# Kernel optimization log

Measured on AMD Instinct MI355X. Metric: run time of the kernel, lower is better.

Reference implementation:

```python
import jax, jax.numpy as jnp
import numpy as np

N_NODES = 50000


def setup_inputs() -> dict:
    key = jax.random.key(0)
    ks = jax.random.split(key, 12)
    node_features = jax.random.normal(ks[0], (50000, 256), dtype=jnp.float32)
    hedge_features = jax.random.normal(ks[1], (25000, 128), dtype=jnp.float32)
    node_senders = jax.random.randint(ks[2], (800000,), 0, 50000, dtype=jnp.int32)
    node_receivers = jnp.sort(jax.random.randint(ks[3], (800000,), 0, 50000, dtype=jnp.int32))
    node_convolution = jax.random.uniform(ks[4], (800000, 1), dtype=jnp.float32)
    hedge2node_senders = jax.random.randint(ks[5], (400000,), 0, 25000, dtype=jnp.int32)
    hedge2node_receivers = jnp.sort(jax.random.randint(ks[6], (400000,), 0, 50000, dtype=jnp.int32))
    hedge2node_convolution = jax.random.uniform(ks[7], (400000, 1), dtype=jnp.float32)
    # Linear params (flax convention: y = x @ W + b, W is [in, out])
    W_msg = jax.random.normal(ks[8], (256, 256), dtype=jnp.float32) / np.sqrt(256.0)
    b_msg = jax.random.normal(ks[9], (256,), dtype=jnp.float32) * 0.01
    W_scale = jax.random.normal(ks[10], (128, 256), dtype=jnp.float32) / np.sqrt(128.0)
    b_scale = jax.random.normal(ks[11], (256,), dtype=jnp.float32) * 0.01
    return {
        "node_features": node_features,
        "hedge_features": hedge_features,
        "node_senders": node_senders,
        "node_receivers": node_receivers,
        "node_convolution": node_convolution,
        "hedge2node_senders": hedge2node_senders,
        "hedge2node_receivers": hedge2node_receivers,
        "hedge2node_convolution": hedge2node_convolution,
        "W_msg": W_msg,
        "b_msg": b_msg,
        "W_scale": W_scale,
        "b_scale": b_scale,
    }


def reference(node_features, hedge_features, node_senders, node_receivers,
              node_convolution, hedge2node_senders, hedge2node_receivers,
              hedge2node_convolution, W_msg, b_msg, W_scale, b_scale):
    # node -> node message pipeline: gather, Linear, per-edge scale, segment_sum
    sender_features = node_features[node_senders]                     # [E, Fin]
    messages = sender_features @ W_msg + b_msg                        # [E, Fout]
    scaled_messages = node_convolution * messages                     # [E, Fout]
    gathered_messages = jax.ops.segment_sum(
        scaled_messages, node_receivers, num_segments=N_NODES)        # [N, Fout]
    # hedge -> node scaling pipeline: gather, Linear, per-edge scale, segment_sum
    hedge_sender_features = hedge_features[hedge2node_senders]        # [E2, Fh]
    hedge_messages = hedge_sender_features @ W_scale + b_scale        # [E2, Fout]
    scaled_hedge_messages = hedge2node_convolution * hedge_messages   # [E2, Fout]
    gathered_scaling = jax.ops.segment_sum(
        scaled_hedge_messages, hedge2node_receivers, num_segments=N_NODES)  # [N, Fout]
    # Hadamard combine
    return gathered_scaling * gathered_messages
```

## Files before the change

### kernel.cpp

```cpp
#include <hip/hip_runtime.h>


typedef __attribute__((ext_vector_type(8))) short bf16x8;
typedef __attribute__((ext_vector_type(4))) float f32x4;

static __device__ __forceinline__ unsigned short f2bf(float f) {
  unsigned u = __float_as_uint(f);
  u += 0x7fff + ((u >> 16) & 1);
  return (unsigned short)(u >> 16);
}
static __device__ __forceinline__ float bf2f(unsigned short h) {
  return __uint_as_float((unsigned)h << 16);
}

__global__ __launch_bounds__(256) void prep_all(
    const float* __restrict__ X, const float* __restrict__ H,
    const int* __restrict__ rcv1, int E1,
    const int* __restrict__ rcv2, int E2, int N,
    const float* __restrict__ Wm, const float* __restrict__ Ws,
    unsigned short* __restrict__ Xb, unsigned short* __restrict__ Hb,
    int* __restrict__ ro1, int* __restrict__ ro2,
    unsigned short* __restrict__ WmT, unsigned short* __restrict__ WsT,
    int nX4, int nH4)
{
  __shared__ float t[32][33];
  const int tid = (int)threadIdx.x;
  int b = (int)blockIdx.x;

  const int bX  = (nX4 + 255) / 256;
  const int bH  = (nH4 + 255) / 256;
  const int bE1 = (E1 + 255) / 256;
  const int bE2 = (E2 + 255) / 256;

  if (b < bX) {
    const int i = b * 256 + tid;
    if (i < nX4) {
      const float4 v = reinterpret_cast<const float4*>(X)[i];
      reinterpret_cast<ushort4*>(Xb)[i] =
          make_ushort4(f2bf(v.x), f2bf(v.y), f2bf(v.z), f2bf(v.w));
    }
    return;
  }
  b -= bX;
  if (b < bH) {
    const int i = b * 256 + tid;
    if (i < nH4) {
      const float4 v = reinterpret_cast<const float4*>(H)[i];
      reinterpret_cast<ushort4*>(Hb)[i] =
          make_ushort4(f2bf(v.x), f2bf(v.y), f2bf(v.z), f2bf(v.w));
    }
    return;
  }
  b -= bH;
  if (b < bE1) {
    const int e = b * 256 + tid;
    if (e < E1) {
      const int c = rcv1[e];
      const int p = (e == 0) ? -1 : rcv1[e - 1];
      for (int n = p + 1; n <= c; ++n) ro1[n] = e;
      if (e == E1 - 1)
        for (int n = c + 1; n <= N; ++n) ro1[n] = E1;
    }
    return;
  }
  b -= bE1;
  if (b < bE2) {
    const int e = b * 256 + tid;
    if (e < E2) {
      const int c = rcv2[e];
      const int p = (e == 0) ? -1 : rcv2[e - 1];
      for (int n = p + 1; n <= c; ++n) ro2[n] = e;
      if (e == E2 - 1)
        for (int n = c + 1; n <= N; ++n) ro2[n] = E2;
    }
    return;
  }
  b -= bE2;
  {
    const float* W; unsigned short* WT; int K, Nn, tile;
    if (b < 64) { W = Wm; WT = WmT; K = 256; Nn = 256; tile = b; }
    else        { W = Ws; WT = WsT; K = 128; Nn = 256; tile = b - 64; }
    const int ntiles_n = Nn / 32;
    const int n0 = (tile % ntiles_n) * 32;
    const int k0 = (tile / ntiles_n) * 32;
    const int tx = tid & 31, ty = tid >> 5;
#pragma unroll
    for (int i = 0; i < 32; i += 8)
      t[ty + i][tx] = W[(size_t)(k0 + ty + i) * Nn + n0 + tx];
    __syncthreads();
#pragma unroll
    for (int i = 0; i < 32; i += 8)
      WT[(size_t)(n0 + ty + i) * K + k0 + tx] = f2bf(t[tx][ty + i]);
  }
}

__global__ __launch_bounds__(256) void scatter_fused(
    const unsigned short* __restrict__ X,
    const int* __restrict__ snd1,
    const float* __restrict__ conv1,
    const int* __restrict__ ro1,
    unsigned short* __restrict__ A,
    float* __restrict__ c1,
    const unsigned short* __restrict__ Hf,
    const int* __restrict__ snd2,
    const float* __restrict__ conv2,
    const int* __restrict__ ro2,
    unsigned short* __restrict__ B,
    float* __restrict__ c2,
    int N)
{
  const int lane = threadIdx.x & 63;
  const int bNode = (N + 3) / 4;
  const int bid = (int)blockIdx.x;

  if (bid < bNode) {
    const int node = __builtin_amdgcn_readfirstlane(
        bid * 4 + ((int)threadIdx.x >> 6));
    if (node >= N) return;
    const int lo = ro1[node];
    const int hi = ro1[node + 1];

    const unsigned short* Xl = X + lane * 4;
    float4 acc = make_float4(0.f, 0.f, 0.f, 0.f);
    float cacc = 0.f;

    int e = lo;
    for (; e + 16 <= hi; e += 16) {
      int s[16]; float cv[16]; ushort4 x[16];
#pragma unroll
      for (int j = 0; j < 16; ++j) s[j] = snd1[e + j];
#pragma unroll
      for (int j = 0; j < 16; ++j) cv[j] = conv1[e + j];
#pragma unroll
      for (int j = 0; j < 16; ++j)
        x[j] = *reinterpret_cast<const ushort4*>(Xl + (size_t)s[j] * 256);
#pragma unroll
      for (int j = 0; j < 16; ++j) {
        acc.x = fmaf(cv[j], bf2f(x[j].x), acc.x);
        acc.y = fmaf(cv[j], bf2f(x[j].y), acc.y);
        acc.z = fmaf(cv[j], bf2f(x[j].z), acc.z);
        acc.w = fmaf(cv[j], bf2f(x[j].w), acc.w);
        cacc += cv[j];
      }
    }
    for (; e + 4 <= hi; e += 4) {
      int s[4]; float cv[4]; ushort4 x[4];
#pragma unroll
      for (int j = 0; j < 4; ++j) s[j] = snd1[e + j];
#pragma unroll
      for (int j = 0; j < 4; ++j) cv[j] = conv1[e + j];
#pragma unroll
      for (int j = 0; j < 4; ++j)
        x[j] = *reinterpret_cast<const ushort4*>(Xl + (size_t)s[j] * 256);
#pragma unroll
      for (int j = 0; j < 4; ++j) {
        acc.x = fmaf(cv[j], bf2f(x[j].x), acc.x);
        acc.y = fmaf(cv[j], bf2f(x[j].y), acc.y);
        acc.z = fmaf(cv[j], bf2f(x[j].z), acc.z);
        acc.w = fmaf(cv[j], bf2f(x[j].w), acc.w);
        cacc += cv[j];
      }
    }
    for (; e < hi; ++e) {
      const int s = snd1[e];
      const float cv = conv1[e];
      const ushort4 x = *reinterpret_cast<const ushort4*>(Xl + (size_t)s * 256);
      acc.x = fmaf(cv, bf2f(x.x), acc.x);
      acc.y = fmaf(cv, bf2f(x.y), acc.y);
      acc.z = fmaf(cv, bf2f(x.z), acc.z);
      acc.w = fmaf(cv, bf2f(x.w), acc.w);
      cacc += cv;
    }

    *reinterpret_cast<ushort4*>(A + (size_t)node * 256 + lane * 4) =
        make_ushort4(f2bf(acc.x), f2bf(acc.y), f2bf(acc.z), f2bf(acc.w));
    if (lane == 0) c1[node] = cacc;
  } else {
    const int node = __builtin_amdgcn_readfirstlane(
        (bid - bNode) * 4 + ((int)threadIdx.x >> 6));
    if (node >= N) return;
    const int lo = ro2[node];
    const int hi = ro2[node + 1];

    const unsigned short* Hl = Hf + lane * 2;
    float2 acc = make_float2(0.f, 0.f);
    float cacc = 0.f;

    int e = lo;
    for (; e + 8 <= hi; e += 8) {
      int s[8]; float cv[8]; ushort2 x[8];
#pragma unroll
      for (int j = 0; j < 8; ++j) s[j] = snd2[e + j];
#pragma unroll
      for (int j = 0; j < 8; ++j) cv[j] = conv2[e + j];
#pragma unroll
      for (int j = 0; j < 8; ++j)
        x[j] = *reinterpret_cast<const ushort2*>(Hl + (size_t)s[j] * 128);
#pragma unroll
      for (int j = 0; j < 8; ++j) {
        acc.x = fmaf(cv[j], bf2f(x[j].x), acc.x);
        acc.y = fmaf(cv[j], bf2f(x[j].y), acc.y);
        cacc += cv[j];
      }
    }
    for (; e < hi; ++e) {
      const int s = snd2[e];
      const float cv = conv2[e];
      const ushort2 x = *reinterpret_cast<const ushort2*>(Hl + (size_t)s * 128);
      acc.x = fmaf(cv, bf2f(x.x), acc.x);
      acc.y = fmaf(cv, bf2f(x.y), acc.y);
      cacc += cv;
    }

    *reinterpret_cast<ushort2*>(B + (size_t)node * 128 + lane * 2) =
        make_ushort2(f2bf(acc.x), f2bf(acc.y));
    if (lane == 0) c2[node] = cacc;
  }
}

__global__ __launch_bounds__(512) void gemm_combine_mfma(
    const unsigned short* __restrict__ A,
    const unsigned short* __restrict__ B,
    const float* __restrict__ c1,
    const float* __restrict__ c2,
    const unsigned short* __restrict__ WmT,
    const float* __restrict__ bm,
    const unsigned short* __restrict__ WsT,
    const float* __restrict__ bs,
    float* __restrict__ out,
    int M)
{
  __shared__ unsigned short lWm[64][264];
  __shared__ unsigned short lWs[64][136];

  const int tid  = (int)threadIdx.x;
  const int lane = tid & 63;
  const int wv   = tid >> 6;
  const int l15  = lane & 15;
  const int lg   = lane >> 4;
  const int m0      = blockIdx.x * 256;
  const int colBlk  = blockIdx.y * 64;

  for (int i = tid; i < 64 * 256 / 8; i += 512) {
    const int c = i >> 5, k8 = (i & 31) << 3;
    *reinterpret_cast<bf16x8*>(&lWm[c][k8]) =
        *reinterpret_cast<const bf16x8*>(WmT + (size_t)(colBlk + c) * 256 + k8);
  }
  for (int i = tid; i < 64 * 128 / 8; i += 512) {
    const int c = i >> 4, k8 = (i & 15) << 3;
    *reinterpret_cast<bf16x8*>(&lWs[c][k8]) =
        *reinterpret_cast<const bf16x8*>(WsT + (size_t)(colBlk + c) * 128 + k8);
  }
  __syncthreads();

  const int rowA = m0 + wv * 32 + l15;

  f32x4 accM[2][4];
  f32x4 accS[2][4];
#pragma unroll
  for (int ms = 0; ms < 2; ++ms)
#pragma unroll
    for (int n = 0; n < 4; ++n) {
      accM[ms][n] = (f32x4)0.f;
      accS[ms][n] = (f32x4)0.f;
    }

#pragma unroll
  for (int kc = 0; kc < 256; kc += 32) {
    const int ko = kc + lg * 8;
    const bf16x8 a0 = *reinterpret_cast<const bf16x8*>(A + (size_t)rowA * 256 + ko);
    const bf16x8 a1 = *reinterpret_cast<const bf16x8*>(A + (size_t)(rowA + 16) * 256 + ko);
#pragma unroll
    for (int n = 0; n < 4; ++n) {
      const bf16x8 w = *reinterpret_cast<const bf16x8*>(&lWm[l15 + n * 16][ko]);
      accM[0][n] = __builtin_amdgcn_mfma_f32_16x16x32_bf16(a0, w, accM[0][n], 0, 0, 0);
      accM[1][n] = __builtin_amdgcn_mfma_f32_16x16x32_bf16(a1, w, accM[1][n], 0, 0, 0);
    }
  }

#pragma unroll
  for (int kc = 0; kc < 128; kc += 32) {
    const int ko = kc + lg * 8;
    const bf16x8 b0 = *reinterpret_cast<const bf16x8*>(B + (size_t)rowA * 128 + ko);
    const bf16x8 b1 = *reinterpret_cast<const bf16x8*>(B + (size_t)(rowA + 16) * 128 + ko);
#pragma unroll
    for (int n = 0; n < 4; ++n) {
      const bf16x8 w = *reinterpret_cast<const bf16x8*>(&lWs[l15 + n * 16][ko]);
      accS[0][n] = __builtin_amdgcn_mfma_f32_16x16x32_bf16(b0, w, accS[0][n], 0, 0, 0);
      accS[1][n] = __builtin_amdgcn_mfma_f32_16x16x32_bf16(b1, w, accS[1][n], 0, 0, 0);
    }
  }

  float bmv[4], bsv[4];
#pragma unroll
  for (int n = 0; n < 4; ++n) {
    bmv[n] = bm[colBlk + n * 16 + l15];
    bsv[n] = bs[colBlk + n * 16 + l15];
  }
#pragma unroll
  for (int ms = 0; ms < 2; ++ms) {
    const int rbase = m0 + wv * 32 + ms * 16 + lg * 4;
#pragma unroll
    for (int r = 0; r < 4; ++r) {
      const int row = rbase + r;
      if (row < M) {
        const float k1 = c1[row];
        const float k2 = c2[row];
#pragma unroll
        for (int n = 0; n < 4; ++n) {
          const int col = colBlk + n * 16 + l15;
          const float mv = accM[ms][n][r] + k1 * bmv[n];
          const float sv = accS[ms][n][r] + k2 * bsv[n];
          out[(size_t)row * 256 + col] = mv * sv;
        }
      }
    }
  }
}

extern "C" void kernel_launch(void* const* d_in, const int* in_sizes, int n_in,
                              void* d_out, int out_size, void* d_ws, size_t ws_size,
                              hipStream_t stream) {
  const float* node_features  = (const float*)d_in[0];
  const float* hedge_features = (const float*)d_in[1];
  const int*   node_senders   = (const int*)d_in[2];
  const int*   node_receivers = (const int*)d_in[3];
  const float* node_conv      = (const float*)d_in[4];
  const int*   h2n_senders    = (const int*)d_in[5];
  const int*   h2n_receivers  = (const int*)d_in[6];
  const float* h2n_conv       = (const float*)d_in[7];
  const float* Wm             = (const float*)d_in[8];
  const float* bm             = (const float*)d_in[9];
  const float* Ws             = (const float*)d_in[10];
  const float* bs             = (const float*)d_in[11];
  float* out = (float*)d_out;

  const int M   = in_sizes[0] / 256;
  const int Nh  = in_sizes[1] / 128;
  const int E   = in_sizes[2];
  const int E2  = in_sizes[5];
  const int Mp  = ((M + 255) / 256) * 256;

  unsigned short* Ab  = (unsigned short*)d_ws;
  unsigned short* Bb  = Ab + (size_t)Mp * 256;
  unsigned short* Xb  = Bb + (size_t)Mp * 128;
  unsigned short* Hb  = Xb + (size_t)M * 256;
  unsigned short* WmT = Hb + (size_t)Nh * 128;
  unsigned short* WsT = WmT + 256 * 256;
  float* c1 = (float*)(WsT + 256 * 128);
  float* c2 = c1 + Mp;
  int*   ro1 = (int*)(c2 + Mp);
  int*   ro2 = ro1 + (M + 1);

  const int nX4 = M * 256 / 4, nH4 = Nh * 128 / 4;
  const int bX  = (nX4 + 255) / 256;
  const int bH  = (nH4 + 255) / 256;
  const int bE1 = (E + 255) / 256;
  const int bE2 = (E2 + 255) / 256;
  const int prep_blocks = bX + bH + bE1 + bE2 + 64 + 32;

  prep_all<<<prep_blocks, 256, 0, stream>>>(
      node_features, hedge_features,
      node_receivers, E, h2n_receivers, E2, M,
      Wm, Ws, Xb, Hb, ro1, ro2, WmT, WsT, nX4, nH4);

  const int bNode = (M + 3) / 4;
  scatter_fused<<<bNode * 2, 256, 0, stream>>>(
      Xb, node_senders, node_conv, ro1, Ab, c1,
      Hb, h2n_senders, h2n_conv, ro2, Bb, c2, M);

  gemm_combine_mfma<<<dim3(Mp / 256, 4), 512, 0, stream>>>(
      Ab, Bb, c1, c2, WmT, bm, WsT, bs, out, M);
}
```

Measured before the change: 134.3 us.

## Slice feature tables by column so each XCD gathers a compact slice

Prep now writes the bf16 node and hedge feature tables in column-sliced layouts: 8 slices of 32 channels for nodes and 2 slices of 64 for hedges. The single fused scatter kernel is split into two kernels. The block index's low bits select the slice, so with round-robin block-to-XCD dispatch each XCD's L2 holds only its own slice. Each wavefront now splits its lanes across several edges at once and reduces them with shuffles. This trades more blocks, narrower loads and extra shuffle reductions for better cache locality in the random gathers.

```diff
diff --git a/kernel.cpp b/kernel.cpp
--- a/kernel.cpp
+++ b/kernel.cpp
@@ -16,9 +16,9 @@
 __global__ __launch_bounds__(256) void prep_all(
     const float* __restrict__ X, const float* __restrict__ H,
     const int* __restrict__ rcv1, int E1,
-    const int* __restrict__ rcv2, int E2, int N,
+    const int* __restrict__ rcv2, int E2, int N, int Nh,
     const float* __restrict__ Wm, const float* __restrict__ Ws,
-    unsigned short* __restrict__ Xb, unsigned short* __restrict__ Hb,
+    unsigned short* __restrict__ Xs, unsigned short* __restrict__ Hs,
     int* __restrict__ ro1, int* __restrict__ ro2,
     unsigned short* __restrict__ WmT, unsigned short* __restrict__ WsT,
     int nX4, int nH4)
@@ -36,7 +36,11 @@
     const int i = b * 256 + tid;
     if (i < nX4) {
       const float4 v = reinterpret_cast<const float4*>(X)[i];
-      reinterpret_cast<ushort4*>(Xb)[i] =
+      const int n = i >> 6, c4 = i & 63;
+      const int slice = c4 >> 3;
+      const int woff = (c4 & 7) * 4;
+      *reinterpret_cast<ushort4*>(
+          Xs + (size_t)slice * N * 32 + (size_t)n * 32 + woff) =
           make_ushort4(f2bf(v.x), f2bf(v.y), f2bf(v.z), f2bf(v.w));
     }
     return;
@@ -46,7 +50,11 @@
     const int i = b * 256 + tid;
     if (i < nH4) {
       const float4 v = reinterpret_cast<const float4*>(H)[i];
-      reinterpret_cast<ushort4*>(Hb)[i] =
+      const int n = i >> 5, c4 = i & 31;
+      const int slice = c4 >> 4;
+      const int woff = (c4 & 15) * 4;
+      *reinterpret_cast<ushort4*>(
+          Hs + (size_t)slice * Nh * 64 + (size_t)n * 64 + woff) =
           make_ushort4(f2bf(v.x), f2bf(v.y), f2bf(v.z), f2bf(v.w));
     }
     return;
@@ -94,127 +102,138 @@
   }
 }
 
-__global__ __launch_bounds__(256) void scatter_fused(
-    const unsigned short* __restrict__ X,
-    const int* __restrict__ snd1,
-    const float* __restrict__ conv1,
-    const int* __restrict__ ro1,
+__global__ __launch_bounds__(256) void scatter_node_xcd(
+    const unsigned short* __restrict__ Xs,
+    const int* __restrict__ snd,
+    const float* __restrict__ conv,
+    const int* __restrict__ ro,
     unsigned short* __restrict__ A,
     float* __restrict__ c1,
-    const unsigned short* __restrict__ Hf,
-    const int* __restrict__ snd2,
-    const float* __restrict__ conv2,
-    const int* __restrict__ ro2,
-    unsigned short* __restrict__ B,
-    float* __restrict__ c2,
     int N)
 {
   const int lane = threadIdx.x & 63;
-  const int bNode = (N + 3) / 4;
   const int bid = (int)blockIdx.x;
-
-  if (bid < bNode) {
-    const int node = __builtin_amdgcn_readfirstlane(
-        bid * 4 + ((int)threadIdx.x >> 6));
-    if (node >= N) return;
-    const int lo = ro1[node];
-    const int hi = ro1[node + 1];
-
-    const unsigned short* Xl = X + lane * 4;
-    float4 acc = make_float4(0.f, 0.f, 0.f, 0.f);
-    float cacc = 0.f;
-
-    int e = lo;
-    for (; e + 16 <= hi; e += 16) {
-      int s[16]; float cv[16]; ushort4 x[16];
-#pragma unroll
-      for (int j = 0; j < 16; ++j) s[j] = snd1[e + j];
-#pragma unroll
-      for (int j = 0; j < 16; ++j) cv[j] = conv1[e + j];
-#pragma unroll
-      for (int j = 0; j < 16; ++j)
-        x[j] = *reinterpret_cast<const ushort4*>(Xl + (size_t)s[j] * 256);
-#pragma unroll
-      for (int j = 0; j < 16; ++j) {
-        acc.x = fmaf(cv[j], bf2f(x[j].x), acc.x);
-        acc.y = fmaf(cv[j], bf2f(x[j].y), acc.y);
-        acc.z = fmaf(cv[j], bf2f(x[j].z), acc.z);
-        acc.w = fmaf(cv[j], bf2f(x[j].w), acc.w);
-        cacc += cv[j];
-      }
-    }
-    for (; e + 4 <= hi; e += 4) {
-      int s[4]; float cv[4]; ushort4 x[4];
-#pragma unroll
-      for (int j = 0; j < 4; ++j) s[j] = snd1[e + j];
-#pragma unroll
-      for (int j = 0; j < 4; ++j) cv[j] = conv1[e + j];
-#pragma unroll
-      for (int j = 0; j < 4; ++j)
-        x[j] = *reinterpret_cast<const ushort4*>(Xl + (size_t)s[j] * 256);
-#pragma unroll
-      for (int j = 0; j < 4; ++j) {
-        acc.x = fmaf(cv[j], bf2f(x[j].x), acc.x);
-        acc.y = fmaf(cv[j], bf2f(x[j].y), acc.y);
-        acc.z = fmaf(cv[j], bf2f(x[j].z), acc.z);
-        acc.w = fmaf(cv[j], bf2f(x[j].w), acc.w);
-        cacc += cv[j];
-      }
-    }
-    for (; e < hi; ++e) {
-      const int s = snd1[e];
-      const float cv = conv1[e];
-      const ushort4 x = *reinterpret_cast<const ushort4*>(Xl + (size_t)s * 256);
-      acc.x = fmaf(cv, bf2f(x.x), acc.x);
-      acc.y = fmaf(cv, bf2f(x.y), acc.y);
-      acc.z = fmaf(cv, bf2f(x.z), acc.z);
-      acc.w = fmaf(cv, bf2f(x.w), acc.w);
-      cacc += cv;
-    }
-
-    *reinterpret_cast<ushort4*>(A + (size_t)node * 256 + lane * 4) =
-        make_ushort4(f2bf(acc.x), f2bf(acc.y), f2bf(acc.z), f2bf(acc.w));
-    if (lane == 0) c1[node] = cacc;
-  } else {
-    const int node = __builtin_amdgcn_readfirstlane(
-        (bid - bNode) * 4 + ((int)threadIdx.x >> 6));
-    if (node >= N) return;
-    const int lo = ro2[node];
-    const int hi = ro2[node + 1];
-
-    const unsigned short* Hl = Hf + lane * 2;
-    float2 acc = make_float2(0.f, 0.f);
-    float cacc = 0.f;
-
-    int e = lo;
-    for (; e + 8 <= hi; e += 8) {
-      int s[8]; float cv[8]; ushort2 x[8];
-#pragma unroll
-      for (int j = 0; j < 8; ++j) s[j] = snd2[e + j];
-#pragma unroll
-      for (int j = 0; j < 8; ++j) cv[j] = conv2[e + j];
-#pragma unroll
-      for (int j = 0; j < 8; ++j)
-        x[j] = *reinterpret_cast<const ushort2*>(Hl + (size_t)s[j] * 128);
-#pragma unroll
-      for (int j = 0; j < 8; ++j) {
-        acc.x = fmaf(cv[j], bf2f(x[j].x), acc.x);
-        acc.y = fmaf(cv[j], bf2f(x[j].y), acc.y);
-        cacc += cv[j];
-      }
-    }
-    for (; e < hi; ++e) {
-      const int s = snd2[e];
-      const float cv = conv2[e];
-      const ushort2 x = *reinterpret_cast<const ushort2*>(Hl + (size_t)s * 128);
-      acc.x = fmaf(cv, bf2f(x.x), acc.x);
-      acc.y = fmaf(cv, bf2f(x.y), acc.y);
-      cacc += cv;
-    }
-
-    *reinterpret_cast<ushort2*>(B + (size_t)node * 128 + lane * 2) =
+  const int slice = bid & 7;
+  const int node = __builtin_amdgcn_readfirstlane(
+      (bid >> 3) * 4 + ((int)threadIdx.x >> 6));
+  if (node >= N) return;
+
+  const int lo = ro[node];
+  const int hi = ro[node + 1];
+
+  const int esub = lane >> 4;
+  const int chp  = lane & 15;
+  const unsigned short* Xsl = Xs + (size_t)slice * N * 32 + chp * 2;
+  const int* sp   = snd + esub;
+  const float* cp = conv + esub;
+
+  float2 acc = make_float2(0.f, 0.f);
+  float cacc = 0.f;
+
+  int e = lo;
+  for (; e + 8 <= hi; e += 8) {
+    const int s0 = sp[e], s1 = sp[e + 4];
+    const float cv0 = cp[e], cv1 = cp[e + 4];
+    const ushort2 x0 = *reinterpret_cast<const ushort2*>(Xsl + (size_t)s0 * 32);
+    const ushort2 x1 = *reinterpret_cast<const ushort2*>(Xsl + (size_t)s1 * 32);
+    acc.x = fmaf(cv0, bf2f(x0.x), acc.x);
+    acc.y = fmaf(cv0, bf2f(x0.y), acc.y);
+    acc.x = fmaf(cv1, bf2f(x1.x), acc.x);
+    acc.y = fmaf(cv1, bf2f(x1.y), acc.y);
+    cacc += cv0 + cv1;
+  }
+  for (; e < hi; e += 4) {
+    const int idx = e + esub;
+    const bool v = idx < hi;
+    const int ic = v ? idx : (hi - 1);
+    const int s = snd[ic];
+    const float cv = v ? conv[ic] : 0.f;
+    const ushort2 x = *reinterpret_cast<const ushort2*>(Xsl + (size_t)s * 32);
+    acc.x = fmaf(cv, bf2f(x.x), acc.x);
+    acc.y = fmaf(cv, bf2f(x.y), acc.y);
+    cacc += cv;
+  }
+
+  acc.x += __shfl_xor(acc.x, 16); acc.x += __shfl_xor(acc.x, 32);
+  acc.y += __shfl_xor(acc.y, 16); acc.y += __shfl_xor(acc.y, 32);
+
+  if (lane < 16) {
+    *reinterpret_cast<ushort2*>(A + (size_t)node * 256 + slice * 32 + chp * 2) =
         make_ushort2(f2bf(acc.x), f2bf(acc.y));
-    if (lane == 0) c2[node] = cacc;
+  }
+  if (slice == 0 && lane == 0) {
+    cacc += __shfl_xor(cacc, 16);
+  }
+  if (slice == 0) {
+    float cs = cacc;
+    cs += __shfl_xor(cs, 16); cs += __shfl_xor(cs, 32);
+    if (lane == 0) c1[node] = cs;
+  }
+}
+
+__global__ __launch_bounds__(256) void scatter_hedge_xcd(
+    const unsigned short* __restrict__ Hs,
+    const int* __restrict__ snd,
+    const float* __restrict__ conv,
+    const int* __restrict__ ro,
+    unsigned short* __restrict__ B,
+    float* __restrict__ c2,
+    int N, int Nh)
+{
+  const int lane = threadIdx.x & 63;
+  const int bid = (int)blockIdx.x;
+  const int slice = bid & 1;
+  const int node = __builtin_amdgcn_readfirstlane(
+      (bid >> 1) * 4 + ((int)threadIdx.x >> 6));
+  if (node >= N) return;
+
+  const int lo = ro[node];
+  const int hi = ro[node + 1];
+
+  const int esub = lane >> 5;
+  const int chp  = lane & 31;
+  const unsigned short* Hl = Hs + (size_t)slice * Nh * 64 + chp * 2;
+  const int* sp   = snd + esub;
+  const float* cp = conv + esub;
+
+  float2 acc = make_float2(0.f, 0.f);
+  float cacc = 0.f;
+
+  int e = lo;
+  for (; e + 4 <= hi; e += 4) {
+    const int s0 = sp[e], s1 = sp[e + 2];
+    const float cv0 = cp[e], cv1 = cp[e + 2];
+    const ushort2 x0 = *reinterpret_cast<const ushort2*>(Hl + (size_t)s0 * 64);
+    const ushort2 x1 = *reinterpret_cast<const ushort2*>(Hl + (size_t)s1 * 64);
+    acc.x = fmaf(cv0, bf2f(x0.x), acc.x);
+    acc.y = fmaf(cv0, bf2f(x0.y), acc.y);
+    acc.x = fmaf(cv1, bf2f(x1.x), acc.x);
+    acc.y = fmaf(cv1, bf2f(x1.y), acc.y);
+    cacc += cv0 + cv1;
+  }
+  for (; e < hi; e += 2) {
+    const int idx = e + esub;
+    const bool v = idx < hi;
+    const int ic = v ? idx : (hi - 1);
+    const int s = snd[ic];
+    const float cv = v ? conv[ic] : 0.f;
+    const ushort2 x = *reinterpret_cast<const ushort2*>(Hl + (size_t)s * 64);
+    acc.x = fmaf(cv, bf2f(x.x), acc.x);
+    acc.y = fmaf(cv, bf2f(x.y), acc.y);
+    cacc += cv;
+  }
+
+  acc.x += __shfl_xor(acc.x, 32);
+  acc.y += __shfl_xor(acc.y, 32);
+
+  if (lane < 32) {
+    *reinterpret_cast<ushort2*>(B + (size_t)node * 128 + slice * 64 + chp * 2) =
+        make_ushort2(f2bf(acc.x), f2bf(acc.y));
+  }
+  if (slice == 0) {
+    float cs = cacc;
+    cs += __shfl_xor(cs, 32);
+    if (lane == 0) c2[node] = cs;
   }
 }
 
@@ -343,9 +362,9 @@
 
   unsigned short* Ab  = (unsigned short*)d_ws;
   unsigned short* Bb  = Ab + (size_t)Mp * 256;
-  unsigned short* Xb  = Bb + (size_t)Mp * 128;
-  unsigned short* Hb  = Xb + (size_t)M * 256;
-  unsigned short* WmT = Hb + (size_t)Nh * 128;
+  unsigned short* Xs  = Bb + (size_t)Mp * 128;
+  unsigned short* Hs  = Xs + (size_t)M * 256;
+  unsigned short* WmT = Hs + (size_t)Nh * 128;
   unsigned short* WsT = WmT + 256 * 256;
   float* c1 = (float*)(WsT + 256 * 128);
   float* c2 = c1 + Mp;
@@ -361,13 +380,14 @@
 
   prep_all<<<prep_blocks, 256, 0, stream>>>(
       node_features, hedge_features,
-      node_receivers, E, h2n_receivers, E2, M,
-      Wm, Ws, Xb, Hb, ro1, ro2, WmT, WsT, nX4, nH4);
-
-  const int bNode = (M + 3) / 4;
-  scatter_fused<<<bNode * 2, 256, 0, stream>>>(
-      Xb, node_senders, node_conv, ro1, Ab, c1,
-      Hb, h2n_senders, h2n_conv, ro2, Bb, c2, M);
+      node_receivers, E, h2n_receivers, E2, M, Nh,
+      Wm, Ws, Xs, Hs, ro1, ro2, WmT, WsT, nX4, nH4);
+
+  const int nodeBlks = (M + 3) / 4;
+  scatter_node_xcd<<<nodeBlks * 8, 256, 0, stream>>>(
+      Xs, node_senders, node_conv, ro1, Ab, c1, M);
+  scatter_hedge_xcd<<<nodeBlks * 2, 256, 0, stream>>>(
+      Hs, h2n_senders, h2n_conv, ro2, Bb, c2, M, Nh);
 
   gemm_combine_mfma<<<dim3(Mp / 256, 4), 512, 0, stream>>>(
       Ab, Bb, c1, c2, WmT, bm, WsT, bs, out, M);
```

Measured after the change: 224.2 us. 66.9% more time.
